# Performance work log

Measured on AMD Instinct MI355X. Metric: run time of the kernel, lower is better.

## Reference

```python
import jax, jax.numpy as jnp
import numpy as np

D_IN, D_K, D_V = 1024, 1024, 1024
B, S = 4, 2048

def setup_inputs() -> dict:
    key = jax.random.key(0)
    ks = jax.random.split(key, 7)
    s = 1.0 / np.sqrt(D_IN)
    return {
        "x": jax.random.normal(ks[0], (B, S, D_IN), dtype=jnp.float32),
        "Wq": jax.random.uniform(ks[1], (D_IN, D_K), jnp.float32, -s, s),
        "bq": jax.random.uniform(ks[2], (D_K,), jnp.float32, -s, s),
        "Wk": jax.random.uniform(ks[3], (D_IN, D_K), jnp.float32, -s, s),
        "bk": jax.random.uniform(ks[4], (D_K,), jnp.float32, -s, s),
        "Wv": jax.random.uniform(ks[5], (D_IN, D_V), jnp.float32, -s, s),
        "bv": jax.random.uniform(ks[6], (D_V,), jnp.float32, -s, s),
    }

def reference(x, Wq, bq, Wk, bk, Wv, bv):
    # QKV projections: [B,S,d_in] @ [d_in,d] + b
    Q = x @ Wq + bq  # [B,S,d_k]
    K = x @ Wk + bk  # [B,S,d_k]
    V = x @ Wv + bv  # [B,S,d_v]
    # Non-standard recipe: softmax over UNSCALED scores, then divide output by sqrt(d_k)
    scores = jnp.einsum('bqd,bkd->bqk', Q, K)  # [B,S,S]
    attn = jax.nn.softmax(scores, axis=2)
    out = jnp.einsum('bqk,bkv->bqv', attn, V) / jnp.sqrt(jnp.asarray(K.shape[2], dtype=x.dtype))
    return out
```

## Files before the change

kernel.cpp:

```cpp
#include <hip/hip_runtime.h>
#include <stdint.h>

typedef unsigned short u16;
typedef _Float16 f16;
typedef _Float16 f16x8 __attribute__((ext_vector_type(8)));
typedef float f32x4 __attribute__((ext_vector_type(4)));

#define DIN 1024
#define SEQ 2048
#define NB 4
#define MB (1u << 20)


__device__ __forceinline__ void gload_lds16(const void* g, void* l) {
    __builtin_amdgcn_global_load_lds(
        (__attribute__((address_space(1))) void*)(uintptr_t)g,
        (__attribute__((address_space(3))) void*)l,
        16, 0, 0);
}

__device__ __forceinline__ int xcd_swz(int h, int cpx) {
    return (h & 7) * cpx + (h >> 3);
}

__device__ __forceinline__ void barrier_raw() {
    asm volatile("" ::: "memory");
    __builtin_amdgcn_s_barrier();
    asm volatile("" ::: "memory");
}
template<int N>
__device__ __forceinline__ void wait_lgkm() {
    asm volatile("s_waitcnt lgkmcnt(%0)" :: "i"(N) : "memory");
    __builtin_amdgcn_sched_barrier(0);
}
template<int N>
__device__ __forceinline__ void wait_vm() {
    asm volatile("s_waitcnt vmcnt(%0)" :: "i"(N) : "memory");
}


__device__ __forceinline__ void gemm256(
    const char* __restrict__ A, const char* __restrict__ B,
    int ldab, int ldbb, int nt, char* smem, f32x4 acc[8][4])
{
    const int tid  = threadIdx.x;
    const int lane = tid & 63;
    const int wave = tid >> 6;
    const int ln15 = lane & 15;
    const int k16  = (lane >> 4) << 4;
    const int wmB  = (wave >> 2) * 128;
    const int wnB  = (wave & 3) * 64;

    #pragma unroll
    for (int m = 0; m < 8; ++m)
        #pragma unroll
        for (int n = 0; n < 4; ++n)
            acc[m][n] = (f32x4){0.f, 0.f, 0.f, 0.f};

    const char* pA[2];
    const char* pB[2];
    #pragma unroll
    for (int i = 0; i < 2; ++i) {
        const int La = i * 8192 + tid * 16;
        const int r  = La >> 7;
        const int sc = (La & 127) ^ ((r & 7) << 4);
        pA[i] = A + (size_t)r * ldab + sc;
        pB[i] = B + (size_t)r * ldbb + sc;
    }
    const int ldsw = wave * 1024;

    f16x8 a0[4][2], a1[4][2], b[4][2];

    auto stage = [&](int g) {
        if (g < 4 * nt) {
            const int ks  = g >> 2;
            const int isB = ((g & 2) == 0);
            const int h   = g & 1;
            char* l = smem + (ks & 1) * 65536 + (isB ? 32768 : 0) + h * 16384 + ldsw;
            #pragma unroll
            for (int i = 0; i < 2; ++i) {
                const char* gp = (isB ? pB[i] + (size_t)(h * 128) * ldbb
                                      : pA[i] + (size_t)(h * 128) * ldab) + ks * 128;
                gload_lds16(gp, l + i * 8192);
            }
        }
    };

#define RDA0(base) { _Pragma("unroll") for (int mf = 0; mf < 4; ++mf) { \
        const int r = wmB + mf * 16 + ln15; \
        const int sw = (r & 7) << 4; \
        const char* p = (base) + r * 128; \
        a0[mf][0] = *(const f16x8*)(p + (k16 ^ sw)); \
        a0[mf][1] = *(const f16x8*)(p + ((64 + k16) ^ sw)); } }

#define RDA1(base) { _Pragma("unroll") for (int mf = 0; mf < 4; ++mf) { \
        const int r = wmB + (mf + 4) * 16 + ln15; \
        const int sw = (r & 7) << 4; \
        const char* p = (base) + r * 128; \
        a1[mf][0] = *(const f16x8*)(p + (k16 ^ sw)); \
        a1[mf][1] = *(const f16x8*)(p + ((64 + k16) ^ sw)); } }

#define RDB2(nf0, base) { _Pragma("unroll") for (int nf = (nf0); nf < (nf0) + 2; ++nf) { \
        const int r = wnB + nf * 16 + ln15; \
        const int sw = (r & 7) << 4; \
        const char* p = (base) + r * 128; \
        b[nf][0] = *(const f16x8*)(p + (k16 ^ sw)); \
        b[nf][1] = *(const f16x8*)(p + ((64 + k16) ^ sw)); } }

#define MM(aa, aoff, nf0) { __builtin_amdgcn_s_setprio(1); \
        _Pragma("unroll") for (int mf = 0; mf < 4; ++mf) \
        _Pragma("unroll") for (int nf = (nf0); nf < (nf0) + 2; ++nf) { \
            acc[(aoff) + mf][nf] = __builtin_amdgcn_mfma_f32_16x16x32_f16( \
                aa[mf][0], b[nf][0], acc[(aoff) + mf][nf], 0, 0, 0); \
            acc[(aoff) + mf][nf] = __builtin_amdgcn_mfma_f32_16x16x32_f16( \
                aa[mf][1], b[nf][1], acc[(aoff) + mf][nf], 0, 0, 0); } \
        __builtin_amdgcn_s_setprio(0); }

    #pragma unroll
    for (int g = 0; g < 8; ++g) stage(g);
    wait_vm<8>();
    barrier_raw();
    RDA0(smem);

    for (int t = 0; t < nt; ++t) {
        const char* sAc = smem + (t & 1) * 65536;
        const char* sBc = sAc + 32768;
        const char* sAn = smem + ((t + 1) & 1) * 65536;
        const int gb = 4 * (t + 2);

        RDB2(0, sBc);
        __builtin_amdgcn_sched_barrier(0);
        RDB2(2, sBc);
        barrier_raw(); wait_lgkm<4>(); MM(a0, 0, 0); barrier_raw();

        RDA1(sAc);
        barrier_raw(); wait_lgkm<8>(); MM(a0, 0, 2); barrier_raw();

        stage(gb + 0); stage(gb + 1);
        if (t < nt - 2) { wait_vm<4>(); } else if (t == nt - 2) { wait_vm<0>(); }
        barrier_raw(); wait_lgkm<0>(); MM(a1, 4, 0); barrier_raw();

        RDA0(sAn);
        stage(gb + 2); stage(gb + 3);
        barrier_raw(); MM(a1, 4, 2); barrier_raw();
    }
#undef RDA0
#undef RDA1
#undef RDB2
#undef MM
}


__device__ __forceinline__ void gemm_tile(
    const char* __restrict__ A, const char* __restrict__ B,
    int lda, int ldb, int ksteps, char* smem, f32x4 acc[4][4])
{
    const int lane = threadIdx.x & 63;
    const int wave = threadIdx.x >> 6;

    #pragma unroll
    for (int m = 0; m < 4; ++m)
        #pragma unroll
        for (int n = 0; n < 4; ++n)
            acc[m][n] = (f32x4){0.f, 0.f, 0.f, 0.f};

    const char* ga[4];
    const char* gb[4];
    int ldsoff[4];
    #pragma unroll
    for (int i = 0; i < 4; ++i) {
        int La = (wave * 4 + i) * 1024 + lane * 16;
        int r  = La >> 7;
        int cb = La & 127;
        int sc = cb ^ ((r & 7) << 4);
        ga[i] = A + (size_t)r * (size_t)(lda * 2) + sc;
        gb[i] = B + (size_t)r * (size_t)(ldb * 2) + sc;
        ldsoff[i] = (wave * 4 + i) * 1024;
    }

    const int wr = (wave >> 1) * 64;
    const int wc = (wave & 1) * 64;

    for (int ks = 0; ks < ksteps; ++ks) {
        #pragma unroll
        for (int i = 0; i < 4; ++i) {
            gload_lds16(ga[i], smem + ldsoff[i]);
            gload_lds16(gb[i], smem + 16384 + ldsoff[i]);
            ga[i] += 128;
            gb[i] += 128;
        }
        __syncthreads();

        #pragma unroll
        for (int kk = 0; kk < 2; ++kk) {
            const int kb = kk * 64 + ((lane >> 4) << 4);
            f16x8 af[4], bfv[4];
            #pragma unroll
            for (int m = 0; m < 4; ++m) {
                int r = wr + m * 16 + (lane & 15);
                af[m] = *(const f16x8*)(smem + r * 128 + (kb ^ ((r & 7) << 4)));
            }
            #pragma unroll
            for (int n = 0; n < 4; ++n) {
                int r = wc + n * 16 + (lane & 15);
                bfv[n] = *(const f16x8*)(smem + 16384 + r * 128 + (kb ^ ((r & 7) << 4)));
            }
            #pragma unroll
            for (int m = 0; m < 4; ++m)
                #pragma unroll
                for (int n = 0; n < 4; ++n)
                    acc[m][n] = __builtin_amdgcn_mfma_f32_16x16x32_f16(
                        af[m], bfv[n], acc[m][n], 0, 0, 0);
        }
        __syncthreads();
    }
}


__global__ __launch_bounds__(256) void k_prep(
    const float* __restrict__ x, f16* __restrict__ xh,
    const float* __restrict__ Wq, const float* __restrict__ Wk,
    const float* __restrict__ Wv, f16* __restrict__ wt)
{
    __shared__ float tile[32][33];
    const int bid = blockIdx.x;
    if (bid < 2048) {
        const int n8 = (NB * SEQ * DIN) / 8;
        for (int idx = bid * 256 + threadIdx.x; idx < n8; idx += 2048 * 256) {
            f32x4 a = ((const f32x4*)x)[(size_t)idx * 2];
            f32x4 b = ((const f32x4*)x)[(size_t)idx * 2 + 1];
            f16x8 o;
            o[0] = (f16)a[0]; o[1] = (f16)a[1]; o[2] = (f16)a[2]; o[3] = (f16)a[3];
            o[4] = (f16)b[0]; o[5] = (f16)b[1]; o[6] = (f16)b[2]; o[7] = (f16)b[3];
            ((f16x8*)xh)[idx] = o;
        }
    } else {
        const int wb = bid - 2048;
        const int mtx = wb >> 10;
        const int rem = wb & 1023;
        const int n0 = (rem & 31) * 32, k0 = (rem >> 5) * 32;
        const float* W = (mtx == 0) ? Wq : (mtx == 1 ? Wk : Wv);
        const int c = threadIdx.x & 31, r0 = threadIdx.x >> 5;
        #pragma unroll
        for (int rr = r0; rr < 32; rr += 8)
            tile[rr][c] = W[(size_t)(k0 + rr) * DIN + n0 + c];
        __syncthreads();
        f16* o = wt + (size_t)mtx * DIN * DIN;
        #pragma unroll
        for (int rr = r0; rr < 32; rr += 8)
            o[(size_t)(n0 + rr) * DIN + k0 + c] = (f16)tile[c][rr];
    }
}

__global__ __launch_bounds__(256) void k_gemm_qkv(
    const f16* __restrict__ xh, const f16* __restrict__ wt,
    const float* __restrict__ bq, const float* __restrict__ bk,
    const float* __restrict__ bv,
    f16* __restrict__ Q, f16* __restrict__ K, f16* __restrict__ Vt)
{
    __shared__ __align__(16) char smem[32768];
    f32x4 acc[4][4];
    const int sid = xcd_swz(blockIdx.x, 192);
    const int blkN = sid % 24;
    const int blkM = sid / 24;
    gemm_tile((const char*)(xh + (size_t)blkM * 128 * DIN),
              (const char*)(wt + (size_t)blkN * 128 * DIN),
              DIN, DIN, DIN / 64, smem, acc);

    const int lane = threadIdx.x & 63;
    const int wave = threadIdx.x >> 6;
    const int row0 = blkM * 128 + (wave >> 1) * 64;
    const int col0 = blkN * 128 + (wave & 1) * 64;

    if (col0 >= 2048) {
        const int bb = row0 >> 11;
        const int sb = row0 & (SEQ - 1);
        f16* Vtb = Vt + (size_t)bb * DIN * SEQ;
        #pragma unroll
        for (int n = 0; n < 4; ++n) {
            int d = (col0 - 2048) + n * 16 + (lane & 15);
            float bias = bv[d];
            #pragma unroll
            for (int m = 0; m < 4; ++m) {
                #pragma unroll
                for (int j = 0; j < 4; ++j) {
                    int s = sb + m * 16 + (lane >> 4) * 4 + j;
                    Vtb[(size_t)d * SEQ + s] = (f16)(acc[m][n][j] + bias);
                }
            }
        }
    } else {
        f16* dst = (col0 < 1024) ? Q : K;
        const float* bsrc = (col0 < 1024) ? bq : bk;
        const int ncb = col0 & 1023;
        #pragma unroll
        for (int n = 0; n < 4; ++n) {
            int nc = ncb + n * 16 + (lane & 15);
            float bias = bsrc[nc];
            #pragma unroll
            for (int m = 0; m < 4; ++m) {
                #pragma unroll
                for (int j = 0; j < 4; ++j) {
                    int row = row0 + m * 16 + (lane >> 4) * 4 + j;
                    dst[(size_t)row * 1024 + nc] = (f16)(acc[m][n][j] + bias);
                }
            }
        }
    }
}

__global__ __launch_bounds__(512, 2) void k_gemm_scores8(
    const f16* __restrict__ Q, const f16* __restrict__ K, f16* __restrict__ S)
{
    extern __shared__ char smem[];
    f32x4 acc[8][4];
    const int sid = xcd_swz(blockIdx.x, 32);
    const int bx = sid & 7, by = (sid >> 3) & 7, b = sid >> 6;
    const f16* Qb = Q + (size_t)b * SEQ * DIN;
    const f16* Kb = K + (size_t)b * SEQ * DIN;
    gemm256((const char*)(Qb + (size_t)by * 256 * DIN),
            (const char*)(Kb + (size_t)bx * 256 * DIN),
            DIN * 2, DIN * 2, DIN / 64, smem, acc);

    f16* Sb = S + (size_t)b * SEQ * SEQ;
    const int lane = threadIdx.x & 63;
    const int wave = threadIdx.x >> 6;
    const int row0 = by * 256 + (wave >> 2) * 128;
    const int col0 = bx * 256 + (wave & 3) * 64;
    #pragma unroll
    for (int m = 0; m < 8; ++m)
        #pragma unroll
        for (int n = 0; n < 4; ++n) {
            int col = col0 + n * 16 + (lane & 15);
            #pragma unroll
            for (int j = 0; j < 4; ++j) {
                int row = row0 + m * 16 + (lane >> 4) * 4 + j;
                Sb[(size_t)row * SEQ + col] = (f16)acc[m][n][j];
            }
        }
}

__global__ __launch_bounds__(256) void k_softmax(
    const f16* __restrict__ S, f16* __restrict__ P)
{
    const size_t row = blockIdx.x;
    const f16* s = S + row * SEQ;
    f16* p = P + row * SEQ;
    const int t = threadIdx.x;

    f16x8 xi = ((const f16x8*)s)[t];
    float v[8];
    #pragma unroll
    for (int j = 0; j < 8; ++j) v[j] = (float)xi[j];

    float mx = v[0];
    #pragma unroll
    for (int j = 1; j < 8; ++j) mx = fmaxf(mx, v[j]);
    #pragma unroll
    for (int o = 32; o; o >>= 1) mx = fmaxf(mx, __shfl_xor(mx, o, 64));
    __shared__ float red[8];
    if ((t & 63) == 0) red[t >> 6] = mx;
    __syncthreads();
    mx = fmaxf(fmaxf(red[0], red[1]), fmaxf(red[2], red[3]));

    float sum = 0.f;
    #pragma unroll
    for (int j = 0; j < 8; ++j) { v[j] = __expf(v[j] - mx); sum += v[j]; }
    #pragma unroll
    for (int o = 32; o; o >>= 1) sum += __shfl_xor(sum, o, 64);
    if ((t & 63) == 0) red[4 + (t >> 6)] = sum;
    __syncthreads();
    sum = (red[4] + red[5]) + (red[6] + red[7]);
    float inv32 = 0.03125f / sum;

    f16x8 o8;
    #pragma unroll
    for (int j = 0; j < 8; ++j) o8[j] = (f16)(v[j] * inv32);
    ((f16x8*)p)[t] = o8;
}

__global__ __launch_bounds__(256) void k_gemm_pv(
    const f16* __restrict__ P, const f16* __restrict__ Vt, float* __restrict__ out)
{
    __shared__ __align__(16) char smem[32768];
    f32x4 acc[4][4];
    const int sid = xcd_swz(blockIdx.x, 64);
    const int bx = sid & 7;
    const int by = (sid >> 3) & 15;
    const int b  = sid >> 7;
    const f16* Pb  = P  + (size_t)b * SEQ * SEQ;
    const f16* Vtb = Vt + (size_t)b * 1024 * SEQ;
    gemm_tile((const char*)(Pb  + (size_t)by * 128 * SEQ),
              (const char*)(Vtb + (size_t)bx * 128 * SEQ),
              SEQ, SEQ, SEQ / 64, smem, acc);

    float* ob = out + (size_t)b * SEQ * 1024;
    const int lane = threadIdx.x & 63;
    const int wave = threadIdx.x >> 6;
    const int row0 = by * 128 + (wave >> 1) * 64;
    const int col0 = bx * 128 + (wave & 1) * 64;
    #pragma unroll
    for (int m = 0; m < 4; ++m)
        #pragma unroll
        for (int n = 0; n < 4; ++n) {
            int col = col0 + n * 16 + (lane & 15);
            #pragma unroll
            for (int j = 0; j < 4; ++j) {
                int row = row0 + m * 16 + (lane >> 4) * 4 + j;
                ob[(size_t)row * 1024 + col] = acc[m][n][j];
            }
        }
}


extern "C" void kernel_launch(void* const* d_in, const int* in_sizes, int n_in,
                              void* d_out, int out_size, void* d_ws, size_t ws_size,
                              hipStream_t stream) {
    const float* x  = (const float*)d_in[0];
    const float* Wq = (const float*)d_in[1];
    const float* bq = (const float*)d_in[2];
    const float* Wk = (const float*)d_in[3];
    const float* bk = (const float*)d_in[4];
    const float* Wv = (const float*)d_in[5];
    const float* bv = (const float*)d_in[6];
    float* out = (float*)d_out;
    char* ws = (char*)d_ws;

    f16*  Q  = (f16*)(ws);
    f16*  K  = (f16*)(ws + (size_t)16 * MB);
    f16*  Vt = (f16*)(ws + (size_t)32 * MB);
    f16*  xh = (f16*)(ws + (size_t)48 * MB);
    f16*  wt = (f16*)(ws + (size_t)64 * MB);
    f16*  S  = (f16*)(ws + (size_t)48 * MB);
    f16*  P  = Q;

    const size_t needed = (size_t)80 * MB;
    if (ws_size < needed) return;

    hipFuncSetAttribute((const void*)k_gemm_scores8,
                        hipFuncAttributeMaxDynamicSharedMemorySize, 131072);

    k_prep<<<5120, 256, 0, stream>>>(x, xh, Wq, Wk, Wv, wt);
    k_gemm_qkv<<<1536, 256, 0, stream>>>(xh, wt, bq, bk, bv, Q, K, Vt);
    k_gemm_scores8<<<256, 512, 131072, stream>>>(Q, K, S);
    k_softmax<<<NB * SEQ, 256, 0, stream>>>(S, P);
    k_gemm_pv<<<512, 256, 0, stream>>>(P, Vt, out);
}
```

Before: 165.9 us.

## Use double-buffered 256x128 pipelined GEMM for QKV and PV kernels

Replaces the simple single-buffered 128x128 GEMM tile used by the QKV projection and PV kernels with an 8-wave, 256x128 tile that double-buffers LDS, prefetches two k-steps ahead via direct global-to-LDS loads, and interleaves LDS fragment reads with MFMA phases under raw barriers and priority hints. This mirrors the scheme already used for the scores GEMM. The aim is to hide global-load latency and increase operand reuse per block. The cost is 96 KB of dynamic LDS per block and fewer, larger blocks per launch, which can hurt tail balance.

```diff
diff --git a/kernel.cpp b/kernel.cpp
--- a/kernel.cpp
+++ b/kernel.cpp
@@ -151,69 +151,123 @@
 }
 
 
-__device__ __forceinline__ void gemm_tile(
+__device__ __forceinline__ void gemm_asym(
     const char* __restrict__ A, const char* __restrict__ B,
-    int lda, int ldb, int ksteps, char* smem, f32x4 acc[4][4])
-{
-    const int lane = threadIdx.x & 63;
-    const int wave = threadIdx.x >> 6;
-
-    #pragma unroll
-    for (int m = 0; m < 4; ++m)
-        #pragma unroll
-        for (int n = 0; n < 4; ++n)
+    int ldab, int ldbb, int nt, char* smem, f32x4 acc[8][2])
+{
+    const int tid  = threadIdx.x;
+    const int lane = tid & 63;
+    const int wave = tid >> 6;
+    const int ln15 = lane & 15;
+    const int k16  = (lane >> 4) << 4;
+    const int wmB  = (wave >> 2) * 128;
+    const int wnB  = (wave & 3) * 32;
+
+    #pragma unroll
+    for (int m = 0; m < 8; ++m)
+        #pragma unroll
+        for (int n = 0; n < 2; ++n)
             acc[m][n] = (f32x4){0.f, 0.f, 0.f, 0.f};
 
-    const char* ga[4];
-    const char* gb[4];
-    int ldsoff[4];
-    #pragma unroll
-    for (int i = 0; i < 4; ++i) {
-        int La = (wave * 4 + i) * 1024 + lane * 16;
-        int r  = La >> 7;
-        int cb = La & 127;
-        int sc = cb ^ ((r & 7) << 4);
-        ga[i] = A + (size_t)r * (size_t)(lda * 2) + sc;
-        gb[i] = B + (size_t)r * (size_t)(ldb * 2) + sc;
-        ldsoff[i] = (wave * 4 + i) * 1024;
-    }
-
-    const int wr = (wave >> 1) * 64;
-    const int wc = (wave & 1) * 64;
-
-    for (int ks = 0; ks < ksteps; ++ks) {
-        #pragma unroll
-        for (int i = 0; i < 4; ++i) {
-            gload_lds16(ga[i], smem + ldsoff[i]);
-            gload_lds16(gb[i], smem + 16384 + ldsoff[i]);
-            ga[i] += 128;
-            gb[i] += 128;
-        }
-        __syncthreads();
-
-        #pragma unroll
-        for (int kk = 0; kk < 2; ++kk) {
-            const int kb = kk * 64 + ((lane >> 4) << 4);
-            f16x8 af[4], bfv[4];
-            #pragma unroll
-            for (int m = 0; m < 4; ++m) {
-                int r = wr + m * 16 + (lane & 15);
-                af[m] = *(const f16x8*)(smem + r * 128 + (kb ^ ((r & 7) << 4)));
+    const char* pA[2];
+    #pragma unroll
+    for (int i = 0; i < 2; ++i) {
+        const int La = i * 8192 + tid * 16;
+        const int r  = La >> 7;
+        const int sc = (La & 127) ^ ((r & 7) << 4);
+        pA[i] = A + (size_t)r * ldab + sc;
+    }
+    const char* pB1;
+    {
+        const int La = tid * 16;
+        const int r  = La >> 7;
+        const int sc = (La & 127) ^ ((r & 7) << 4);
+        pB1 = B + (size_t)r * ldbb + sc;
+    }
+    const int ldsw = wave * 1024;
+
+    f16x8 a0[4][2], a1[4][2], b[2][2];
+
+    auto stage = [&](int g) {
+        if (g < 4 * nt) {
+            const int ks = g >> 2;
+            const int u  = g & 3;
+            char* bufb = smem + (ks & 1) * 49152;
+            if (u < 2) {
+                gload_lds16(pB1 + (size_t)(u * 64) * ldbb + ks * 128,
+                            bufb + 32768 + u * 8192 + ldsw);
+            } else {
+                const int h = u - 2;
+                char* l = bufb + h * 16384 + ldsw;
+                gload_lds16(pA[0] + (size_t)(h * 128) * ldab + ks * 128, l);
+                gload_lds16(pA[1] + (size_t)(h * 128) * ldab + ks * 128, l + 8192);
             }
-            #pragma unroll
-            for (int n = 0; n < 4; ++n) {
-                int r = wc + n * 16 + (lane & 15);
-                bfv[n] = *(const f16x8*)(smem + 16384 + r * 128 + (kb ^ ((r & 7) << 4)));
-            }
-            #pragma unroll
-            for (int m = 0; m < 4; ++m)
-                #pragma unroll
-                for (int n = 0; n < 4; ++n)
-                    acc[m][n] = __builtin_amdgcn_mfma_f32_16x16x32_f16(
-                        af[m], bfv[n], acc[m][n], 0, 0, 0);
-        }
-        __syncthreads();
-    }
+        }
+    };
+
+#define ARDA0(base) { _Pragma("unroll") for (int mf = 0; mf < 4; ++mf) { \
+        const int r = wmB + mf * 16 + ln15; \
+        const int sw = (r & 7) << 4; \
+        const char* p = (base) + r * 128; \
+        a0[mf][0] = *(const f16x8*)(p + (k16 ^ sw)); \
+        a0[mf][1] = *(const f16x8*)(p + ((64 + k16) ^ sw)); } }
+
+#define ARDA1(base) { _Pragma("unroll") for (int mf = 0; mf < 4; ++mf) { \
+        const int r = wmB + (mf + 4) * 16 + ln15; \
+        const int sw = (r & 7) << 4; \
+        const char* p = (base) + r * 128; \
+        a1[mf][0] = *(const f16x8*)(p + (k16 ^ sw)); \
+        a1[mf][1] = *(const f16x8*)(p + ((64 + k16) ^ sw)); } }
+
+#define ARDB(base) { \
+        { const int r = wnB + ln15; const int sw = (r & 7) << 4; \
+          const char* p = (base) + r * 128; \
+          b[0][0] = *(const f16x8*)(p + (k16 ^ sw)); \
+          b[0][1] = *(const f16x8*)(p + ((64 + k16) ^ sw)); } \
+        __builtin_amdgcn_sched_barrier(0); \
+        { const int r = wnB + 16 + ln15; const int sw = (r & 7) << 4; \
+          const char* p = (base) + r * 128; \
+          b[1][0] = *(const f16x8*)(p + (k16 ^ sw)); \
+          b[1][1] = *(const f16x8*)(p + ((64 + k16) ^ sw)); } }
+
+#define AMM(aa, aoff, nf) { __builtin_amdgcn_s_setprio(1); \
+        _Pragma("unroll") for (int mf = 0; mf < 4; ++mf) { \
+            acc[(aoff) + mf][nf] = __builtin_amdgcn_mfma_f32_16x16x32_f16( \
+                aa[mf][0], b[nf][0], acc[(aoff) + mf][nf], 0, 0, 0); \
+            acc[(aoff) + mf][nf] = __builtin_amdgcn_mfma_f32_16x16x32_f16( \
+                aa[mf][1], b[nf][1], acc[(aoff) + mf][nf], 0, 0, 0); } \
+        __builtin_amdgcn_s_setprio(0); }
+
+    #pragma unroll
+    for (int g = 0; g < 8; ++g) stage(g);
+    wait_vm<6>();
+    barrier_raw();
+    ARDA0(smem);
+
+    for (int t = 0; t < nt; ++t) {
+        const char* sAc = smem + (t & 1) * 49152;
+        const char* sBc = sAc + 32768;
+        const char* sAn = smem + ((t + 1) & 1) * 49152;
+        const int gb = 4 * (t + 2);
+
+        ARDB(sBc);
+        barrier_raw(); wait_lgkm<2>(); AMM(a0, 0, 0); barrier_raw();
+
+        ARDA1(sAc);
+        barrier_raw(); wait_lgkm<8>(); AMM(a0, 0, 1); barrier_raw();
+
+        stage(gb + 0); stage(gb + 1);
+        if (t < nt - 2) { wait_vm<2>(); } else if (t == nt - 2) { wait_vm<0>(); }
+        barrier_raw(); wait_lgkm<0>(); AMM(a1, 4, 0); barrier_raw();
+
+        ARDA0(sAn);
+        stage(gb + 2); stage(gb + 3);
+        barrier_raw(); AMM(a1, 4, 1); barrier_raw();
+    }
+#undef ARDA0
+#undef ARDA1
+#undef ARDB
+#undef AMM
 }
 
 
@@ -252,36 +306,36 @@
     }
 }
 
-__global__ __launch_bounds__(256) void k_gemm_qkv(
+__global__ __launch_bounds__(512, 2) void k_gemm_qkv8(
     const f16* __restrict__ xh, const f16* __restrict__ wt,
     const float* __restrict__ bq, const float* __restrict__ bk,
     const float* __restrict__ bv,
     f16* __restrict__ Q, f16* __restrict__ K, f16* __restrict__ Vt)
 {
-    __shared__ __align__(16) char smem[32768];
-    f32x4 acc[4][4];
-    const int sid = xcd_swz(blockIdx.x, 192);
+    extern __shared__ char smem[];
+    f32x4 acc[8][2];
+    const int sid = xcd_swz(blockIdx.x, 96);
     const int blkN = sid % 24;
     const int blkM = sid / 24;
-    gemm_tile((const char*)(xh + (size_t)blkM * 128 * DIN),
+    gemm_asym((const char*)(xh + (size_t)blkM * 256 * DIN),
               (const char*)(wt + (size_t)blkN * 128 * DIN),
-              DIN, DIN, DIN / 64, smem, acc);
+              DIN * 2, DIN * 2, DIN / 64, smem, acc);
 
     const int lane = threadIdx.x & 63;
     const int wave = threadIdx.x >> 6;
-    const int row0 = blkM * 128 + (wave >> 1) * 64;
-    const int col0 = blkN * 128 + (wave & 1) * 64;
+    const int row0 = blkM * 256 + (wave >> 2) * 128;
+    const int col0 = blkN * 128 + (wave & 3) * 32;
 
     if (col0 >= 2048) {
         const int bb = row0 >> 11;
         const int sb = row0 & (SEQ - 1);
         f16* Vtb = Vt + (size_t)bb * DIN * SEQ;
         #pragma unroll
-        for (int n = 0; n < 4; ++n) {
+        for (int n = 0; n < 2; ++n) {
             int d = (col0 - 2048) + n * 16 + (lane & 15);
             float bias = bv[d];
             #pragma unroll
-            for (int m = 0; m < 4; ++m) {
+            for (int m = 0; m < 8; ++m) {
                 #pragma unroll
                 for (int j = 0; j < 4; ++j) {
                     int s = sb + m * 16 + (lane >> 4) * 4 + j;
@@ -294,11 +348,11 @@
         const float* bsrc = (col0 < 1024) ? bq : bk;
         const int ncb = col0 & 1023;
         #pragma unroll
-        for (int n = 0; n < 4; ++n) {
+        for (int n = 0; n < 2; ++n) {
             int nc = ncb + n * 16 + (lane & 15);
             float bias = bsrc[nc];
             #pragma unroll
-            for (int m = 0; m < 4; ++m) {
+            for (int m = 0; m < 8; ++m) {
                 #pragma unroll
                 for (int j = 0; j < 4; ++j) {
                     int row = row0 + m * 16 + (lane >> 4) * 4 + j;
@@ -379,30 +433,30 @@
     ((f16x8*)p)[t] = o8;
 }
 
-__global__ __launch_bounds__(256) void k_gemm_pv(
+__global__ __launch_bounds__(512, 2) void k_gemm_pv8(
     const f16* __restrict__ P, const f16* __restrict__ Vt, float* __restrict__ out)
 {
-    __shared__ __align__(16) char smem[32768];
-    f32x4 acc[4][4];
-    const int sid = xcd_swz(blockIdx.x, 64);
+    extern __shared__ char smem[];
+    f32x4 acc[8][2];
+    const int sid = xcd_swz(blockIdx.x, 32);
     const int bx = sid & 7;
-    const int by = (sid >> 3) & 15;
-    const int b  = sid >> 7;
+    const int by = (sid >> 3) & 7;
+    const int b  = sid >> 6;
     const f16* Pb  = P  + (size_t)b * SEQ * SEQ;
     const f16* Vtb = Vt + (size_t)b * 1024 * SEQ;
-    gemm_tile((const char*)(Pb  + (size_t)by * 128 * SEQ),
+    gemm_asym((const char*)(Pb  + (size_t)by * 256 * SEQ),
               (const char*)(Vtb + (size_t)bx * 128 * SEQ),
-              SEQ, SEQ, SEQ / 64, smem, acc);
+              SEQ * 2, SEQ * 2, SEQ / 64, smem, acc);
 
     float* ob = out + (size_t)b * SEQ * 1024;
     const int lane = threadIdx.x & 63;
     const int wave = threadIdx.x >> 6;
-    const int row0 = by * 128 + (wave >> 1) * 64;
-    const int col0 = bx * 128 + (wave & 1) * 64;
-    #pragma unroll
-    for (int m = 0; m < 4; ++m)
-        #pragma unroll
-        for (int n = 0; n < 4; ++n) {
+    const int row0 = by * 256 + (wave >> 2) * 128;
+    const int col0 = bx * 128 + (wave & 3) * 32;
+    #pragma unroll
+    for (int m = 0; m < 8; ++m)
+        #pragma unroll
+        for (int n = 0; n < 2; ++n) {
             int col = col0 + n * 16 + (lane & 15);
             #pragma unroll
             for (int j = 0; j < 4; ++j) {
@@ -437,12 +491,16 @@
     const size_t needed = (size_t)80 * MB;
     if (ws_size < needed) return;
 
+    hipFuncSetAttribute((const void*)k_gemm_qkv8,
+                        hipFuncAttributeMaxDynamicSharedMemorySize, 98304);
     hipFuncSetAttribute((const void*)k_gemm_scores8,
                         hipFuncAttributeMaxDynamicSharedMemorySize, 131072);
+    hipFuncSetAttribute((const void*)k_gemm_pv8,
+                        hipFuncAttributeMaxDynamicSharedMemorySize, 98304);
 
     k_prep<<<5120, 256, 0, stream>>>(x, xh, Wq, Wk, Wv, wt);
-    k_gemm_qkv<<<1536, 256, 0, stream>>>(xh, wt, bq, bk, bv, Q, K, Vt);
+    k_gemm_qkv8<<<768, 512, 98304, stream>>>(xh, wt, bq, bk, bv, Q, K, Vt);
     k_gemm_scores8<<<256, 512, 131072, stream>>>(Q, K, S);
     k_softmax<<<NB * SEQ, 256, 0, stream>>>(S, P);
-    k_gemm_pv<<<512, 256, 0, stream>>>(P, Vt, out);
-}
+    k_gemm_pv8<<<256, 512, 98304, stream>>>(P, Vt, out);
+}
```

Measured after the change: 175.7 us. 1.06x slower.

## Split QKV projection into 256-tile QK GEMM and separate V GEMM, regroup PV blocks

Applied to the files above, without the earlier changes.

The fused QKV projection GEMM with 128x128 tiles is split in two. Q and K now come from the larger 256x256-tile gemm256 kernel (512 threads, 128KB dynamic LDS), which reuses data better per tile. V keeps the 128-tile kernel with its transposed store. Separately, the PV GEMM block-to-tile mapping is changed so each XCD works on 2x4 tile groups, which should improve L2 sharing of P and Vt rows. The cost is one extra kernel launch, and the 256-block QK grid may underfill the CUs.

```diff
diff --git a/kernel.cpp b/kernel.cpp
--- a/kernel.cpp
+++ b/kernel.cpp
@@ -252,58 +252,73 @@
     }
 }
 
-__global__ __launch_bounds__(256) void k_gemm_qkv(
+__global__ __launch_bounds__(512, 2) void k_gemm_qk8(
     const f16* __restrict__ xh, const f16* __restrict__ wt,
     const float* __restrict__ bq, const float* __restrict__ bk,
-    const float* __restrict__ bv,
-    f16* __restrict__ Q, f16* __restrict__ K, f16* __restrict__ Vt)
+    f16* __restrict__ Q, f16* __restrict__ K)
+{
+    extern __shared__ char smem[];
+    f32x4 acc[8][4];
+    const int sid = xcd_swz(blockIdx.x, 32);
+    const int blkN = sid & 7;
+    const int blkM = sid >> 3;
+    gemm256((const char*)(xh + (size_t)blkM * 256 * DIN),
+            (const char*)(wt + (size_t)blkN * 256 * DIN),
+            DIN * 2, DIN * 2, DIN / 64, smem, acc);
+
+    const int lane = threadIdx.x & 63;
+    const int wave = threadIdx.x >> 6;
+    const int row0 = blkM * 256 + (wave >> 2) * 128;
+    const int col0 = blkN * 256 + (wave & 3) * 64;
+
+    f16* dst = (col0 < 1024) ? Q : K;
+    const float* bsrc = (col0 < 1024) ? bq : bk;
+    const int ncb = col0 & 1023;
+    #pragma unroll
+    for (int n = 0; n < 4; ++n) {
+        int nc = ncb + n * 16 + (lane & 15);
+        float bias = bsrc[nc];
+        #pragma unroll
+        for (int m = 0; m < 8; ++m) {
+            #pragma unroll
+            for (int j = 0; j < 4; ++j) {
+                int row = row0 + m * 16 + (lane >> 4) * 4 + j;
+                dst[(size_t)row * 1024 + nc] = (f16)(acc[m][n][j] + bias);
+            }
+        }
+    }
+}
+
+__global__ __launch_bounds__(256) void k_gemm_v(
+    const f16* __restrict__ xh, const f16* __restrict__ wtv,
+    const float* __restrict__ bv, f16* __restrict__ Vt)
 {
     __shared__ __align__(16) char smem[32768];
     f32x4 acc[4][4];
-    const int sid = xcd_swz(blockIdx.x, 192);
-    const int blkN = sid % 24;
-    const int blkM = sid / 24;
-    gemm_tile((const char*)(xh + (size_t)blkM * 128 * DIN),
-              (const char*)(wt + (size_t)blkN * 128 * DIN),
+    const int sid = xcd_swz(blockIdx.x, 64);
+    const int blkN = sid & 7;
+    const int blkM = sid >> 3;
+    gemm_tile((const char*)(xh  + (size_t)blkM * 128 * DIN),
+              (const char*)(wtv + (size_t)blkN * 128 * DIN),
               DIN, DIN, DIN / 64, smem, acc);
 
     const int lane = threadIdx.x & 63;
     const int wave = threadIdx.x >> 6;
     const int row0 = blkM * 128 + (wave >> 1) * 64;
     const int col0 = blkN * 128 + (wave & 1) * 64;
-
-    if (col0 >= 2048) {
-        const int bb = row0 >> 11;
-        const int sb = row0 & (SEQ - 1);
-        f16* Vtb = Vt + (size_t)bb * DIN * SEQ;
-        #pragma unroll
-        for (int n = 0; n < 4; ++n) {
-            int d = (col0 - 2048) + n * 16 + (lane & 15);
-            float bias = bv[d];
-            #pragma unroll
-            for (int m = 0; m < 4; ++m) {
-                #pragma unroll
-                for (int j = 0; j < 4; ++j) {
-                    int s = sb + m * 16 + (lane >> 4) * 4 + j;
-                    Vtb[(size_t)d * SEQ + s] = (f16)(acc[m][n][j] + bias);
-                }
-            }
-        }
-    } else {
-        f16* dst = (col0 < 1024) ? Q : K;
-        const float* bsrc = (col0 < 1024) ? bq : bk;
-        const int ncb = col0 & 1023;
-        #pragma unroll
-        for (int n = 0; n < 4; ++n) {
-            int nc = ncb + n * 16 + (lane & 15);
-            float bias = bsrc[nc];
-            #pragma unroll
-            for (int m = 0; m < 4; ++m) {
-                #pragma unroll
-                for (int j = 0; j < 4; ++j) {
-                    int row = row0 + m * 16 + (lane >> 4) * 4 + j;
-                    dst[(size_t)row * 1024 + nc] = (f16)(acc[m][n][j] + bias);
-                }
+    const int bb = row0 >> 11;
+    const int sb = row0 & (SEQ - 1);
+    f16* Vtb = Vt + (size_t)bb * DIN * SEQ;
+    #pragma unroll
+    for (int n = 0; n < 4; ++n) {
+        int d = col0 + n * 16 + (lane & 15);
+        float bias = bv[d];
+        #pragma unroll
+        for (int m = 0; m < 4; ++m) {
+            #pragma unroll
+            for (int j = 0; j < 4; ++j) {
+                int s = sb + m * 16 + (lane >> 4) * 4 + j;
+                Vtb[(size_t)d * SEQ + s] = (f16)(acc[m][n][j] + bias);
             }
         }
     }
@@ -384,10 +399,13 @@
 {
     __shared__ __align__(16) char smem[32768];
     f32x4 acc[4][4];
-    const int sid = xcd_swz(blockIdx.x, 64);
-    const int bx = sid & 7;
-    const int by = (sid >> 3) & 15;
-    const int b  = sid >> 7;
+    const int xcd = blockIdx.x & 7;
+    const int idx = blockIdx.x >> 3;
+    const int c   = xcd * 8 + idx / 8;
+    const int t   = idx % 8;
+    const int b   = c >> 4;
+    const int by  = ((c >> 1) & 7) * 2 + t / 4;
+    const int bx  = (c & 1) * 4 + t % 4;
     const f16* Pb  = P  + (size_t)b * SEQ * SEQ;
     const f16* Vtb = Vt + (size_t)b * 1024 * SEQ;
     gemm_tile((const char*)(Pb  + (size_t)by * 128 * SEQ),
@@ -437,11 +455,14 @@
     const size_t needed = (size_t)80 * MB;
     if (ws_size < needed) return;
 
+    hipFuncSetAttribute((const void*)k_gemm_qk8,
+                        hipFuncAttributeMaxDynamicSharedMemorySize, 131072);
     hipFuncSetAttribute((const void*)k_gemm_scores8,
                         hipFuncAttributeMaxDynamicSharedMemorySize, 131072);
 
     k_prep<<<5120, 256, 0, stream>>>(x, xh, Wq, Wk, Wv, wt);
-    k_gemm_qkv<<<1536, 256, 0, stream>>>(xh, wt, bq, bk, bv, Q, K, Vt);
+    k_gemm_qk8<<<256, 512, 131072, stream>>>(xh, wt, bq, bk, Q, K);
+    k_gemm_v<<<512, 256, 0, stream>>>(xh, wt + (size_t)2048 * DIN, bv, Vt);
     k_gemm_scores8<<<256, 512, 131072, stream>>>(Q, K, S);
     k_softmax<<<NB * SEQ, 256, 0, stream>>>(S, P);
     k_gemm_pv<<<512, 256, 0, stream>>>(P, Vt, out);
```

Result: no change. 163.6 us (-1.4%).
